# Kernel optimization log

Measured on AMD Instinct MI355X. Metric: run time of the kernel, lower is better.

The kernel has to match this reference:

```python
import jax, jax.numpy as jnp
import numpy as np

N_BUS = 4096
BATCH = 1024


def setup_inputs() -> dict:
    key = jax.random.key(0)
    ks = jax.random.split(key, 10)
    u = jax.random.normal(ks[0], (BATCH, N_BUS), dtype=jnp.float32)
    w = jax.random.normal(ks[1], (BATCH, N_BUS), dtype=jnp.float32)
    # parameters (torch.rand -> uniform[0,1); Linear init ~ U(-1/sqrt(n), 1/sqrt(n)))
    G = jax.random.uniform(ks[2], (N_BUS, N_BUS), dtype=jnp.float32)
    B = jax.random.uniform(ks[3], (N_BUS, N_BUS), dtype=jnp.float32)
    bias_p = jax.random.uniform(ks[4], (1, N_BUS), dtype=jnp.float32)
    bias_q = jax.random.uniform(ks[5], (1, N_BUS), dtype=jnp.float32)
    lim = 1.0 / np.sqrt(N_BUS)
    Wp = jax.random.uniform(ks[6], (N_BUS, N_BUS), dtype=jnp.float32, minval=-lim, maxval=lim)
    bp = jax.random.uniform(ks[7], (N_BUS,), dtype=jnp.float32, minval=-lim, maxval=lim)
    Wq = jax.random.uniform(ks[8], (N_BUS, N_BUS), dtype=jnp.float32, minval=-lim, maxval=lim)
    bq = jax.random.uniform(ks[9], (N_BUS,), dtype=jnp.float32, minval=-lim, maxval=lim)
    return {"u": u, "w": w, "G": G, "B": B, "bias_p": bias_p, "bias_q": bias_q,
            "Wp": Wp, "bp": bp, "Wq": Wq, "bq": bq}


def reference(u, w, G, B, bias_p, bias_q, Wp, bp, Wq, bq):
    # Algebraically identical to the original's outer-product form:
    # p_i = sum_k (u_i u_k + w_i w_k) G_ik + (w_i u_k - u_i w_k) B_ik
    #     = u_i (G u)_i + w_i (G w)_i + w_i (B u)_i - u_i (B w)_i
    # q_i = sum_k (w_i u_k - u_i w_k) G_ik - (u_i u_k + w_i w_k) B_ik
    #     = w_i (G u)_i - u_i (G w)_i - u_i (B u)_i - w_i (B w)_i
    Gu = u @ G.T  # (batch, n_bus): (G u)_i = sum_k G_ik u_k
    Gw = w @ G.T
    Bu = u @ B.T
    Bw = w @ B.T
    p = u * Gu + w * Gw + w * Bu - u * Bw + bias_p
    q = w * Gu - u * Gw - u * Bu - w * Bw + bias_q
    # nn.Linear: y = x @ W^T + b
    p = p @ Wp.T + bp
    q = q @ Wq.T + bq
    return (p, q)
```

## Files before the change

kernel.cpp:

```cpp
#include <hip/hip_runtime.h>
#include <hip/hip_bf16.h>

#define NB 4096
#define MB 1024
#define SZ ((size_t)MB * NB)
#define NN ((size_t)NB * NB)

typedef __bf16 bf16_t;
typedef __attribute__((ext_vector_type(8))) __bf16 bf16x8;
typedef __attribute__((ext_vector_type(4))) float f32x4;
typedef __attribute__((ext_vector_type(4))) unsigned int u32x4;

#define AS1 __attribute__((address_space(1)))
#define AS3 __attribute__((address_space(3)))
#define GLOAD16(gp, lp)                                                        \
  __builtin_amdgcn_global_load_lds((const AS1 unsigned int*)(gp),              \
                                   (AS3 unsigned int*)(lp), 16, 0, 0)
#define SBAR() __builtin_amdgcn_s_barrier()
#define SCHEDB() __builtin_amdgcn_sched_barrier(0)
#define MFMA16(a, b, c) __builtin_amdgcn_mfma_f32_16x16x32_bf16((a), (b), (c), 0, 0, 0)
#define VMCNT(n) asm volatile("s_waitcnt vmcnt(" #n ")" ::: "memory")


__device__ __forceinline__ bf16x8 neg8(bf16x8 x) {
  u32x4 t;
  __builtin_memcpy(&t, &x, 16);
  t ^= 0x80008000u;
  bf16x8 y;
  __builtin_memcpy(&y, &t, 16);
  return y;
}

__device__ __forceinline__ bf16x8 cvt8(float4 a, float4 b) {
  bf16x8 v;
  v[0] = (bf16_t)a.x; v[1] = (bf16_t)a.y; v[2] = (bf16_t)a.z; v[3] = (bf16_t)a.w;
  v[4] = (bf16_t)b.x; v[5] = (bf16_t)b.y; v[6] = (bf16_t)b.z; v[7] = (bf16_t)b.w;
  return v;
}

#define ITEM_S (SZ / 8)
#define ITEM_N (NN / 8)

__global__ __launch_bounds__(256) void prep6_kernel(
    const float* __restrict__ u, const float* __restrict__ w,
    const float* __restrict__ G, const float* __restrict__ Bm,
    const float* __restrict__ Wp, const float* __restrict__ Wq,
    bf16_t* __restrict__ ws) {
  size_t stride = (size_t)gridDim.x * blockDim.x;
  const size_t tot = 2 * ITEM_S + 4 * ITEM_N;
  for (size_t i = (size_t)blockIdx.x * blockDim.x + threadIdx.x; i < tot;
       i += stride) {
    const float* src;
    bf16_t* dst;
    size_t off;
    if (i < ITEM_S) { src = u; dst = ws; off = i; }
    else if (i < 2 * ITEM_S) { src = w; dst = ws + SZ; off = i - ITEM_S; }
    else if (i < 2 * ITEM_S + ITEM_N) { src = G; dst = ws + 2 * SZ; off = i - 2 * ITEM_S; }
    else if (i < 2 * ITEM_S + 2 * ITEM_N) { src = Bm; dst = ws + 2 * SZ + NN; off = i - 2 * ITEM_S - ITEM_N; }
    else if (i < 2 * ITEM_S + 3 * ITEM_N) { src = Wp; dst = ws + 2 * SZ + 2 * NN; off = i - 2 * ITEM_S - 2 * ITEM_N; }
    else { src = Wq; dst = ws + 2 * SZ + 3 * NN; off = i - 2 * ITEM_S - 3 * ITEM_N; }
    const float4* s = reinterpret_cast<const float4*>(src) + off * 2;
    reinterpret_cast<bf16x8*>(dst)[off] = cvt8(s[0], s[1]);
  }
}

__global__ __launch_bounds__(256) void prep4_kernel(
    const float* __restrict__ u, const float* __restrict__ w,
    const float* __restrict__ G, const float* __restrict__ Bm,
    bf16_t* __restrict__ ws) {
  size_t stride = (size_t)gridDim.x * blockDim.x;
  const size_t tot = 2 * ITEM_S + 2 * ITEM_N;
  for (size_t i = (size_t)blockIdx.x * blockDim.x + threadIdx.x; i < tot;
       i += stride) {
    const float* src;
    bf16_t* dst;
    size_t off;
    if (i < ITEM_S) { src = u; dst = ws; off = i; }
    else if (i < 2 * ITEM_S) { src = w; dst = ws + SZ; off = i - ITEM_S; }
    else if (i < 2 * ITEM_S + ITEM_N) { src = G; dst = ws + 2 * SZ; off = i - 2 * ITEM_S; }
    else { src = Bm; dst = ws + 2 * SZ + NN; off = i - 2 * ITEM_S - ITEM_N; }
    const float4* s = reinterpret_cast<const float4*>(src) + off * 2;
    reinterpret_cast<bf16x8*>(dst)[off] = cvt8(s[0], s[1]);
  }
}

__global__ __launch_bounds__(256, 1) void fused1_v10(
    const float* __restrict__ u, const float* __restrict__ w,
    const bf16_t* __restrict__ ubf, const bf16_t* __restrict__ wbf,
    const bf16_t* __restrict__ Gbf, const bf16_t* __restrict__ Bbf,
    const float* __restrict__ bias_p, const float* __restrict__ bias_q,
    bf16_t* __restrict__ pq) {
  __shared__ bf16_t lds[4][4][128 * 32];
  const int tid = threadIdx.x, lane = tid & 63, wv = tid >> 6;
  const int bid = blockIdx.x;
  const int t = (bid & 7) * 32 + (bid >> 3);
  const int row0 = (t & 7) * 128, col0 = (t >> 3) * 128;
  const int wm = (wv >> 1) * 64, wn = (wv & 1) * 64;
  const int lr = lane & 15, kq = lane >> 4;
  const int kswz = (kq ^ ((lr >> 1) & 3)) << 3;

  const int srow = tid >> 2;
  const int sc = (tid & 3) ^ ((tid >> 3) & 3);
  const bf16_t* gsA[4];
  const bf16_t* gsB[4];
  {
    const bf16_t* bases[4] = {ubf, wbf, Gbf, Bbf};
    const int r0s[4] = {row0, row0, col0, col0};
#pragma unroll
    for (int o = 0; o < 4; ++o) {
      gsA[o] = bases[o] + (size_t)(r0s[o] + srow) * NB + sc * 8;
      gsB[o] = gsA[o] + (size_t)64 * NB;
    }
  }

#define F1_ISSUE(hh)                                                          \
  do {                                                                        \
    const int _sl = (hh) & 3;                                                 \
    const int _ko = (hh) * 32;                                                \
    _Pragma("unroll") for (int _o = 0; _o < 4; ++_o) {                        \
      GLOAD16(gsA[_o] + _ko, &lds[_sl][_o][wv * 512]);                        \
      GLOAD16(gsB[_o] + _ko, &lds[_sl][_o][2048 + wv * 512]);                 \
    }                                                                         \
  } while (0)

  int aoff[4], boff[4];
#pragma unroll
  for (int m = 0; m < 4; ++m) aoff[m] = (wm + m * 16 + lr) * 32 + kswz;
#pragma unroll
  for (int n = 0; n < 4; ++n) boff[n] = (wn + n * 16 + lr) * 32 + kswz;

  f32x4 aS[4][4] = {}, aT[4][4] = {};

  F1_ISSUE(0); F1_ISSUE(1); F1_ISSUE(2);
  VMCNT(16);
  SBAR();
  SCHEDB();

  for (int h = 0; h < 128; ++h) {
    const int slot = h & 3;
    bf16x8 au[4], aw[4], bG[4], bB[4];
#pragma unroll
    for (int m = 0; m < 4; ++m) {
      au[m] = *reinterpret_cast<const bf16x8*>(&lds[slot][0][aoff[m]]);
      aw[m] = *reinterpret_cast<const bf16x8*>(&lds[slot][1][aoff[m]]);
    }
#pragma unroll
    for (int n = 0; n < 4; ++n) {
      bG[n] = *reinterpret_cast<const bf16x8*>(&lds[slot][2][boff[n]]);
      bB[n] = *reinterpret_cast<const bf16x8*>(&lds[slot][3][boff[n]]);
    }
    if (h + 3 < 128) F1_ISSUE(h + 3);
#pragma unroll
    for (int n = 0; n < 4; ++n) {
      bf16x8 bn = neg8(bB[n]);
#pragma unroll
      for (int m = 0; m < 4; ++m) {
        aS[m][n] = MFMA16(au[m], bG[n], aS[m][n]);
        aS[m][n] = MFMA16(aw[m], bn, aS[m][n]);
        aT[m][n] = MFMA16(aw[m], bG[n], aT[m][n]);
        aT[m][n] = MFMA16(au[m], bB[n], aT[m][n]);
      }
    }
    if (h <= 124) {
      VMCNT(16);
      SBAR();
      SCHEDB();
    } else if (h == 125) {
      VMCNT(8);
      SBAR();
      SCHEDB();
    } else if (h == 126) {
      VMCNT(0);
      SBAR();
      SCHEDB();
    }
  }

  const int fr = lane & 15, fq = kq;
#pragma unroll
  for (int m = 0; m < 4; ++m)
#pragma unroll
    for (int n = 0; n < 4; ++n)
#pragma unroll
      for (int j = 0; j < 4; ++j) {
        int r = row0 + wm + m * 16 + fq * 4 + j;
        int c = col0 + wn + n * 16 + fr;
        size_t idx = (size_t)r * NB + c;
        float U = u[idx], W = w[idx];
        float S = aS[m][n][j], T = aT[m][n][j];
        pq[idx] = (bf16_t)(U * S + W * T + bias_p[c]);
        pq[SZ + idx] = (bf16_t)(W * S - U * T + bias_q[c]);
      }
}

__global__ __launch_bounds__(256, 2) void gemm2_v9(
    const bf16_t* __restrict__ pq, const bf16_t* __restrict__ Wpb,
    const bf16_t* __restrict__ Wqb, const float* __restrict__ bp,
    const float* __restrict__ bq, float* __restrict__ out) {
  __shared__ bf16_t lds[4][2][128 * 32];
  const int tid = threadIdx.x, lane = tid & 63, wv = tid >> 6;
  const int bid = blockIdx.x;
  const int t = (bid & 7) * 64 + (bid >> 3);
  const int z = t >> 8;
  const int s = t & 255;
  const int row0 = (s & 7) * 128, col0 = (s >> 3) * 128;
  const int koff = (bid & 1) << 6;

  const bf16_t* A = pq + (size_t)z * SZ;
  const bf16_t* Wm = z ? Wqb : Wpb;
  const float* bias = z ? bq : bp;
  float* C = out + (size_t)z * SZ;

  const int wm = (wv >> 1) * 64, wn = (wv & 1) * 64;
  const int lr = lane & 15, kq = lane >> 4;
  const int kswz = (kq ^ ((lr >> 1) & 3)) << 3;

  const int srow = tid >> 2;
  const int sc = (tid & 3) ^ ((tid >> 3) & 3);
  const bf16_t* gA0 = A + (size_t)(row0 + srow) * NB + sc * 8;
  const bf16_t* gA1 = gA0 + (size_t)64 * NB;
  const bf16_t* gW0 = Wm + (size_t)(col0 + srow) * NB + sc * 8;
  const bf16_t* gW1 = gW0 + (size_t)64 * NB;

#define G2_ISSUE(hh)                                                           \
  do {                                                                         \
    const int _sl = (hh) & 3;                                                  \
    const int _ko = (((hh) + koff) & 127) * 32;                                \
    GLOAD16(gA0 + _ko, &lds[_sl][0][wv * 512]);                                \
    GLOAD16(gA1 + _ko, &lds[_sl][0][2048 + wv * 512]);                         \
    GLOAD16(gW0 + _ko, &lds[_sl][1][wv * 512]);                                \
    GLOAD16(gW1 + _ko, &lds[_sl][1][2048 + wv * 512]);                         \
  } while (0)

  int aoff[4], woff[4];
#pragma unroll
  for (int m = 0; m < 4; ++m) aoff[m] = (wm + m * 16 + lr) * 32 + kswz;
#pragma unroll
  for (int n = 0; n < 4; ++n) woff[n] = (wn + n * 16 + lr) * 32 + kswz;

  f32x4 acc[4][4] = {};

  G2_ISSUE(0); G2_ISSUE(1); G2_ISSUE(2);
  VMCNT(4);
  SBAR();
  SCHEDB();

  const int HTOT = 2 * (NB / 64);
  for (int h = 0; h < HTOT; ++h) {
    const int slot = h & 3;
    const bool pf = (h + 3) < HTOT;

    bf16x8 av[4], bw[4];
#pragma unroll
    for (int m = 0; m < 4; ++m)
      av[m] = *reinterpret_cast<const bf16x8*>(&lds[slot][0][aoff[m]]);
#pragma unroll
    for (int n = 0; n < 4; ++n)
      bw[n] = *reinterpret_cast<const bf16x8*>(&lds[slot][1][woff[n]]);
    if (pf) G2_ISSUE(h + 3);
#pragma unroll
    for (int m = 0; m < 4; ++m)
#pragma unroll
      for (int n = 0; n < 4; ++n)
        acc[m][n] = MFMA16(av[m], bw[n], acc[m][n]);
    if (h < HTOT - 3)
      VMCNT(4);
    else if (h == HTOT - 3)
      VMCNT(2);
    else if (h == HTOT - 2)
      VMCNT(0);
    SBAR();
    SCHEDB();
  }

  const int fr = lane & 15, fq = kq;
#pragma unroll
  for (int m = 0; m < 4; ++m)
#pragma unroll
    for (int n = 0; n < 4; ++n)
#pragma unroll
      for (int j = 0; j < 4; ++j) {
        int r = row0 + wm + m * 16 + fq * 4 + j;
        int c = col0 + wn + n * 16 + fr;
        C[(size_t)r * NB + c] = acc[m][n][j] + bias[c];
      }
}

__device__ __forceinline__ int swz_off32(int r, int kk) {
  return r * 32 + ((kk ^ ((r >> 1) & 3)) << 3);
}

__device__ __forceinline__ void fb_stage_f32(const float* __restrict__ src,
                                             int row0, int k0, bf16_t* lds, int t) {
  int r = t >> 2, kk = t & 3;
  const float* p = src + (size_t)(row0 + r) * NB + k0 + (kk << 3);
  float4 v0 = *reinterpret_cast<const float4*>(p);
  float4 v1 = *reinterpret_cast<const float4*>(p + 4);
  *reinterpret_cast<bf16x8*>(lds + swz_off32(r, kk)) = cvt8(v0, v1);
}

__global__ __launch_bounds__(256, 2) void fb_gemm2(
    const bf16_t* __restrict__ pq, const float* __restrict__ Wp,
    const float* __restrict__ Wq, const float* __restrict__ bp,
    const float* __restrict__ bq, float* __restrict__ out) {
  __shared__ bf16_t lA[128 * 32], lW[128 * 32];
  const int z = blockIdx.z;
  const bf16_t* A = pq + (size_t)z * SZ;
  const float* Wm = z ? Wq : Wp;
  const float* bias = z ? bq : bp;
  float* C = out + (size_t)z * SZ;
  const int tid = threadIdx.x;
  const int lane = tid & 63, wv = tid >> 6;
  const int wm = (wv >> 1) * 64, wn = (wv & 1) * 64;
  const int row0 = blockIdx.y * 128, col0 = blockIdx.x * 128;
  const int lr = lane & 15, kq = lane >> 4;
  const int fslot = (kq ^ ((lr >> 1) & 3)) << 3;
  f32x4 acc[4][4] = {};
  for (int kt = 0; kt < NB; kt += 32) {
#pragma unroll
    for (int p = 0; p < 2; ++p) {
      int cb = p * 256 + wv * 64;
      int ci = cb + lane;
      int r = ci >> 2, kl = ci & 3;
      int ks = kl ^ ((r >> 1) & 3);
      const bf16_t* g = A + (size_t)(row0 + r) * NB + kt + (ks << 3);
      GLOAD16(g, lA + cb * 8);
    }
#pragma unroll
    for (int p = 0; p < 2; ++p)
      fb_stage_f32(Wm, col0, kt, lW, p * 256 + tid);
    __syncthreads();
    bf16x8 af[4], bg[4];
#pragma unroll
    for (int m = 0; m < 4; ++m)
      af[m] = *reinterpret_cast<const bf16x8*>(lA + (wm + m * 16 + lr) * 32 + fslot);
#pragma unroll
    for (int n = 0; n < 4; ++n)
      bg[n] = *reinterpret_cast<const bf16x8*>(lW + (wn + n * 16 + lr) * 32 + fslot);
#pragma unroll
    for (int m = 0; m < 4; ++m)
#pragma unroll
      for (int n = 0; n < 4; ++n)
        acc[m][n] = MFMA16(af[m], bg[n], acc[m][n]);
    __syncthreads();
  }
  const int fr = lane & 15, fq = lane >> 4;
#pragma unroll
  for (int m = 0; m < 4; ++m)
#pragma unroll
    for (int n = 0; n < 4; ++n)
#pragma unroll
      for (int j = 0; j < 4; ++j) {
        int r = row0 + wm + m * 16 + fq * 4 + j;
        int c = col0 + wn + n * 16 + fr;
        C[(size_t)r * NB + c] = acc[m][n][j] + bias[c];
      }
}

__global__ __launch_bounds__(512, 2) void fb_fused1(
    const float* __restrict__ u, const float* __restrict__ w,
    const float* __restrict__ G, const float* __restrict__ Bm,
    const float* __restrict__ bias_p, const float* __restrict__ bias_q,
    bf16_t* __restrict__ pq) {
  __shared__ bf16_t lU[128 * 32], lW[128 * 32], lG[128 * 32], lB[128 * 32];
  const int tid = threadIdx.x;
  const int lane = tid & 63, wv = tid >> 6;
  const int wm = (wv >> 2) * 64, wn = (wv & 3) * 32;
  const int row0 = blockIdx.y * 128, col0 = blockIdx.x * 128;
  const int lr = lane & 15, kq = lane >> 4;
  const int fslot = (kq ^ ((lr >> 1) & 3)) << 3;
  f32x4 aS[4][2] = {}, aT[4][2] = {};
  for (int kt = 0; kt < NB; kt += 32) {
    fb_stage_f32(u, row0, kt, lU, tid);
    fb_stage_f32(w, row0, kt, lW, tid);
    fb_stage_f32(G, col0, kt, lG, tid);
    fb_stage_f32(Bm, col0, kt, lB, tid);
    __syncthreads();
    bf16x8 au[4], aw[4], bG[2], bB[2], bBn[2];
#pragma unroll
    for (int m = 0; m < 4; ++m) {
      int off = (wm + m * 16 + lr) * 32 + fslot;
      au[m] = *reinterpret_cast<const bf16x8*>(lU + off);
      aw[m] = *reinterpret_cast<const bf16x8*>(lW + off);
    }
#pragma unroll
    for (int n = 0; n < 2; ++n) {
      int off = (wn + n * 16 + lr) * 32 + fslot;
      bG[n] = *reinterpret_cast<const bf16x8*>(lG + off);
      bB[n] = *reinterpret_cast<const bf16x8*>(lB + off);
      bBn[n] = neg8(bB[n]);
    }
#pragma unroll
    for (int m = 0; m < 4; ++m)
#pragma unroll
      for (int n = 0; n < 2; ++n) {
        aS[m][n] = MFMA16(au[m], bG[n], aS[m][n]);
        aS[m][n] = MFMA16(aw[m], bBn[n], aS[m][n]);
        aT[m][n] = MFMA16(aw[m], bG[n], aT[m][n]);
        aT[m][n] = MFMA16(au[m], bB[n], aT[m][n]);
      }
    __syncthreads();
  }
  const int fr = lane & 15, fq = lane >> 4;
#pragma unroll
  for (int m = 0; m < 4; ++m)
#pragma unroll
    for (int n = 0; n < 2; ++n)
#pragma unroll
      for (int j = 0; j < 4; ++j) {
        int r = row0 + wm + m * 16 + fq * 4 + j;
        int c = col0 + wn + n * 16 + fr;
        size_t idx = (size_t)r * NB + c;
        float U = u[idx], W = w[idx];
        float S = aS[m][n][j], T = aT[m][n][j];
        pq[idx] = (bf16_t)(U * S + W * T + bias_p[c]);
        pq[SZ + idx] = (bf16_t)(W * S - U * T + bias_q[c]);
      }
}

extern "C" void kernel_launch(void* const* d_in, const int* in_sizes, int n_in,
                              void* d_out, int out_size, void* d_ws, size_t ws_size,
                              hipStream_t stream) {
  const float* u = (const float*)d_in[0];
  const float* w = (const float*)d_in[1];
  const float* G = (const float*)d_in[2];
  const float* Bm = (const float*)d_in[3];
  const float* bias_p = (const float*)d_in[4];
  const float* bias_q = (const float*)d_in[5];
  const float* Wp = (const float*)d_in[6];
  const float* bp = (const float*)d_in[7];
  const float* Wq = (const float*)d_in[8];
  const float* bq = (const float*)d_in[9];
  (void)in_sizes; (void)n_in; (void)out_size;

  const size_t need_full = (6 * SZ + 4 * NN) * sizeof(bf16_t);
  const size_t need_mid = (6 * SZ + 2 * NN) * sizeof(bf16_t);

  if (ws_size >= need_full) {
    bf16_t* ws = (bf16_t*)d_ws;
    bf16_t* ubf = ws;
    bf16_t* wbf = ws + SZ;
    bf16_t* Gbf = ws + 2 * SZ;
    bf16_t* Bbf = Gbf + NN;
    bf16_t* Wpb = Bbf + NN;
    bf16_t* Wqb = Wpb + NN;
    bf16_t* pqw = Wqb + NN;
    prep6_kernel<<<2048, 256, 0, stream>>>(u, w, G, Bm, Wp, Wq, ws);
    fused1_v10<<<256, 256, 0, stream>>>(u, w, ubf, wbf, Gbf, Bbf,
                                        bias_p, bias_q, pqw);
    gemm2_v9<<<512, 256, 0, stream>>>(pqw, Wpb, Wqb, bp, bq, (float*)d_out);
  } else if (ws_size >= need_mid) {
    bf16_t* ws = (bf16_t*)d_ws;
    bf16_t* ubf = ws;
    bf16_t* wbf = ws + SZ;
    bf16_t* Gbf = ws + 2 * SZ;
    bf16_t* Bbf = Gbf + NN;
    bf16_t* pqw = Bbf + NN;
    prep4_kernel<<<2048, 256, 0, stream>>>(u, w, G, Bm, ws);
    fused1_v10<<<256, 256, 0, stream>>>(u, w, ubf, wbf, Gbf, Bbf,
                                        bias_p, bias_q, pqw);
    fb_gemm2<<<dim3(NB / 128, MB / 128, 2), 256, 0, stream>>>(
        pqw, Wp, Wq, bp, bq, (float*)d_out);
  } else {
    bf16_t* pqw = (bf16_t*)d_ws;
    fb_fused1<<<dim3(NB / 128, MB / 128), 512, 0, stream>>>(
        u, w, G, Bm, bias_p, bias_q, pqw);
    fb_gemm2<<<dim3(NB / 128, MB / 128, 2), 256, 0, stream>>>(
        pqw, Wp, Wq, bp, bq, (float*)d_out);
  }
}
```

Baseline: 308.3 us.

## Switch fused first GEMM to 32x32 MFMA with 8 waves per block

Rewrites the fused first-stage kernel to use 32x32x16 bf16 MFMA instructions instead of 16x16x32, with 512 threads (8 waves) per block, each wave owning a 64x32 output sub-tile. Each thread now issues one async global-to-LDS load per operand per stage instead of two, and the epilogue hoists the bias loads. The aim is fewer LDS reads per FLOP and more waves to hide latency. The risk is higher register pressure from the 16-wide accumulators and different bank-conflict behaviour under the existing swizzle.

```diff
diff --git a/kernel.cpp b/kernel.cpp
--- a/kernel.cpp
+++ b/kernel.cpp
@@ -9,6 +9,7 @@
 typedef __bf16 bf16_t;
 typedef __attribute__((ext_vector_type(8))) __bf16 bf16x8;
 typedef __attribute__((ext_vector_type(4))) float f32x4;
+typedef __attribute__((ext_vector_type(16))) float f32x16;
 typedef __attribute__((ext_vector_type(4))) unsigned int u32x4;
 
 #define AS1 __attribute__((address_space(1)))
@@ -19,6 +20,7 @@
 #define SBAR() __builtin_amdgcn_s_barrier()
 #define SCHEDB() __builtin_amdgcn_sched_barrier(0)
 #define MFMA16(a, b, c) __builtin_amdgcn_mfma_f32_16x16x32_bf16((a), (b), (c), 0, 0, 0)
+#define MFMA32(a, b, c) __builtin_amdgcn_mfma_f32_32x32x16_bf16((a), (b), (c), 0, 0, 0)
 #define VMCNT(n) asm volatile("s_waitcnt vmcnt(" #n ")" ::: "memory")
 
 
@@ -84,7 +86,7 @@
   }
 }
 
-__global__ __launch_bounds__(256, 1) void fused1_v10(
+__global__ __launch_bounds__(512, 2) void fused1_v11(
     const float* __restrict__ u, const float* __restrict__ w,
     const bf16_t* __restrict__ ubf, const bf16_t* __restrict__ wbf,
     const bf16_t* __restrict__ Gbf, const bf16_t* __restrict__ Bbf,
@@ -95,102 +97,100 @@
   const int bid = blockIdx.x;
   const int t = (bid & 7) * 32 + (bid >> 3);
   const int row0 = (t & 7) * 128, col0 = (t >> 3) * 128;
-  const int wm = (wv >> 1) * 64, wn = (wv & 1) * 64;
-  const int lr = lane & 15, kq = lane >> 4;
-  const int kswz = (kq ^ ((lr >> 1) & 3)) << 3;
-
-  const int srow = tid >> 2;
-  const int sc = (tid & 3) ^ ((tid >> 3) & 3);
-  const bf16_t* gsA[4];
-  const bf16_t* gsB[4];
-  {
-    const bf16_t* bases[4] = {ubf, wbf, Gbf, Bbf};
-    const int r0s[4] = {row0, row0, col0, col0};
-#pragma unroll
-    for (int o = 0; o < 4; ++o) {
-      gsA[o] = bases[o] + (size_t)(r0s[o] + srow) * NB + sc * 8;
-      gsB[o] = gsA[o] + (size_t)64 * NB;
-    }
-  }
-
-#define F1_ISSUE(hh)                                                          \
-  do {                                                                        \
-    const int _sl = (hh) & 3;                                                 \
-    const int _ko = (hh) * 32;                                                \
-    _Pragma("unroll") for (int _o = 0; _o < 4; ++_o) {                        \
-      GLOAD16(gsA[_o] + _ko, &lds[_sl][_o][wv * 512]);                        \
-      GLOAD16(gsB[_o] + _ko, &lds[_sl][_o][2048 + wv * 512]);                 \
-    }                                                                         \
-  } while (0)
-
-  int aoff[4], boff[4];
-#pragma unroll
-  for (int m = 0; m < 4; ++m) aoff[m] = (wm + m * 16 + lr) * 32 + kswz;
-#pragma unroll
-  for (int n = 0; n < 4; ++n) boff[n] = (wn + n * 16 + lr) * 32 + kswz;
-
-  f32x4 aS[4][4] = {}, aT[4][4] = {};
-
-  F1_ISSUE(0); F1_ISSUE(1); F1_ISSUE(2);
-  VMCNT(16);
+  const int wm = (wv >> 2) * 64, wn = (wv & 3) * 32;
+  const int lr32 = lane & 31, hi = lane >> 5;
+  const int sw = (lr32 >> 1) & 3;
+
+  const int srow = wv * 16 + (lane >> 2);
+  const int sc = (lane & 3) ^ ((lane >> 3) & 3);
+  const bf16_t* gsrc[4];
+  gsrc[0] = ubf + (size_t)(row0 + srow) * NB + sc * 8;
+  gsrc[1] = wbf + (size_t)(row0 + srow) * NB + sc * 8;
+  gsrc[2] = Gbf + (size_t)(col0 + srow) * NB + sc * 8;
+  gsrc[3] = Bbf + (size_t)(col0 + srow) * NB + sc * 8;
+
+#define F1_ISS(op, sl, ko) GLOAD16(gsrc[op] + (ko), &lds[sl][op][wv * 512])
+
+  int kchunk[2];
+#pragma unroll
+  for (int kk = 0; kk < 2; ++kk) kchunk[kk] = (((kk * 2 + hi) ^ sw) << 3);
+  int aoff[2];
+#pragma unroll
+  for (int mi = 0; mi < 2; ++mi) aoff[mi] = (wm + mi * 32 + lr32) * 32;
+  const int boff = (wn + lr32) * 32;
+
+  f32x16 aS[2] = {}, aT[2] = {};
+
+#pragma unroll
+  for (int hh = 0; hh < 3; ++hh) {
+    F1_ISS(0, hh, hh * 32);
+    F1_ISS(1, hh, hh * 32);
+    F1_ISS(2, hh, hh * 32);
+    F1_ISS(3, hh, hh * 32);
+  }
+  VMCNT(8);
   SBAR();
   SCHEDB();
 
-  for (int h = 0; h < 128; ++h) {
+  const int HTOT = 128;
+  for (int h = 0; h < HTOT; ++h) {
     const int slot = h & 3;
-    bf16x8 au[4], aw[4], bG[4], bB[4];
-#pragma unroll
-    for (int m = 0; m < 4; ++m) {
-      au[m] = *reinterpret_cast<const bf16x8*>(&lds[slot][0][aoff[m]]);
-      aw[m] = *reinterpret_cast<const bf16x8*>(&lds[slot][1][aoff[m]]);
-    }
-#pragma unroll
-    for (int n = 0; n < 4; ++n) {
-      bG[n] = *reinterpret_cast<const bf16x8*>(&lds[slot][2][boff[n]]);
-      bB[n] = *reinterpret_cast<const bf16x8*>(&lds[slot][3][boff[n]]);
-    }
-    if (h + 3 < 128) F1_ISSUE(h + 3);
-#pragma unroll
-    for (int n = 0; n < 4; ++n) {
-      bf16x8 bn = neg8(bB[n]);
-#pragma unroll
-      for (int m = 0; m < 4; ++m) {
-        aS[m][n] = MFMA16(au[m], bG[n], aS[m][n]);
-        aS[m][n] = MFMA16(aw[m], bn, aS[m][n]);
-        aT[m][n] = MFMA16(aw[m], bG[n], aT[m][n]);
-        aT[m][n] = MFMA16(au[m], bB[n], aT[m][n]);
-      }
-    }
-    if (h <= 124) {
-      VMCNT(16);
-      SBAR();
-      SCHEDB();
-    } else if (h == 125) {
+    const bool pf = (h + 3) < HTOT;
+    const int pslot = (h + 3) & 3;
+    const int pko = (h + 3) * 32;
+
+    bf16x8 bG[2], bB[2], au[2][2], aw[2][2];
+#pragma unroll
+    for (int kk = 0; kk < 2; ++kk) {
+      bG[kk] = *reinterpret_cast<const bf16x8*>(&lds[slot][2][boff + kchunk[kk]]);
+      bB[kk] = *reinterpret_cast<const bf16x8*>(&lds[slot][3][boff + kchunk[kk]]);
+#pragma unroll
+      for (int mi = 0; mi < 2; ++mi) {
+        au[mi][kk] = *reinterpret_cast<const bf16x8*>(&lds[slot][0][aoff[mi] + kchunk[kk]]);
+        aw[mi][kk] = *reinterpret_cast<const bf16x8*>(&lds[slot][1][aoff[mi] + kchunk[kk]]);
+      }
+    }
+    if (pf) {
+      F1_ISS(0, pslot, pko);
+      F1_ISS(1, pslot, pko);
+      F1_ISS(2, pslot, pko);
+      F1_ISS(3, pslot, pko);
+    }
+#pragma unroll
+    for (int kk = 0; kk < 2; ++kk) {
+      bf16x8 bn = neg8(bB[kk]);
+#pragma unroll
+      for (int mi = 0; mi < 2; ++mi) {
+        aS[mi] = MFMA32(au[mi][kk], bG[kk], aS[mi]);
+        aS[mi] = MFMA32(aw[mi][kk], bn, aS[mi]);
+        aT[mi] = MFMA32(aw[mi][kk], bG[kk], aT[mi]);
+        aT[mi] = MFMA32(au[mi][kk], bB[kk], aT[mi]);
+      }
+    }
+    if (h < HTOT - 3)
       VMCNT(8);
-      SBAR();
-      SCHEDB();
-    } else if (h == 126) {
+    else if (h == HTOT - 3)
+      VMCNT(4);
+    else if (h == HTOT - 2)
       VMCNT(0);
-      SBAR();
-      SCHEDB();
-    }
-  }
-
-  const int fr = lane & 15, fq = kq;
-#pragma unroll
-  for (int m = 0; m < 4; ++m)
-#pragma unroll
-    for (int n = 0; n < 4; ++n)
-#pragma unroll
-      for (int j = 0; j < 4; ++j) {
-        int r = row0 + wm + m * 16 + fq * 4 + j;
-        int c = col0 + wn + n * 16 + fr;
-        size_t idx = (size_t)r * NB + c;
-        float U = u[idx], W = w[idx];
-        float S = aS[m][n][j], T = aT[m][n][j];
-        pq[idx] = (bf16_t)(U * S + W * T + bias_p[c]);
-        pq[SZ + idx] = (bf16_t)(W * S - U * T + bias_q[c]);
-      }
+    SBAR();
+    SCHEDB();
+  }
+
+  const int c = col0 + wn + lr32;
+  const float bp_ = bias_p[c], bq_ = bias_q[c];
+#pragma unroll
+  for (int mi = 0; mi < 2; ++mi) {
+#pragma unroll
+    for (int j = 0; j < 16; ++j) {
+      int r = row0 + wm + mi * 32 + (j & 3) + 8 * (j >> 2) + 4 * hi;
+      size_t idx = (size_t)r * NB + c;
+      float U = u[idx], W = w[idx];
+      float S = aS[mi][j], T = aT[mi][j];
+      pq[idx] = (bf16_t)(U * S + W * T + bp_);
+      pq[SZ + idx] = (bf16_t)(W * S - U * T + bq_);
+    }
+  }
 }
 
 __global__ __launch_bounds__(256, 2) void gemm2_v9(
@@ -446,7 +446,7 @@
     bf16_t* Wqb = Wpb + NN;
     bf16_t* pqw = Wqb + NN;
     prep6_kernel<<<2048, 256, 0, stream>>>(u, w, G, Bm, Wp, Wq, ws);
-    fused1_v10<<<256, 256, 0, stream>>>(u, w, ubf, wbf, Gbf, Bbf,
+    fused1_v11<<<256, 512, 0, stream>>>(u, w, ubf, wbf, Gbf, Bbf,
                                         bias_p, bias_q, pqw);
     gemm2_v9<<<512, 256, 0, stream>>>(pqw, Wpb, Wqb, bp, bq, (float*)d_out);
   } else if (ws_size >= need_mid) {
@@ -457,7 +457,7 @@
     bf16_t* Bbf = Gbf + NN;
     bf16_t* pqw = Bbf + NN;
     prep4_kernel<<<2048, 256, 0, stream>>>(u, w, G, Bm, ws);
-    fused1_v10<<<256, 256, 0, stream>>>(u, w, ubf, wbf, Gbf, Bbf,
+    fused1_v11<<<256, 512, 0, stream>>>(u, w, ubf, wbf, Gbf, Bbf,
                                         bias_p, bias_q, pqw);
     fb_gemm2<<<dim3(NB / 128, MB / 128, 2), 256, 0, stream>>>(
         pqw, Wp, Wq, bp, bq, (float*)d_out);
```

Result: no change. 308.9 us (+0.2%).
